# Optimization experiments

Hardware: AMD Instinct MI355X
Metric: run time of the kernel (lower is better)

## Reference

```python
import jax, jax.numpy as jnp
import numpy as np

DIM = 768
NUM_HEADS = 12
HEAD_DIM = DIM // NUM_HEADS
B, V, L = 1, 8, 512


def _block_mask_bias(V, L, dtype):
    # allowed[v_q, v_k]: views 0,1 attend to views 0,1 (incl. self); views >=2 causal (v_q >= v_k)
    vq = jnp.arange(V)[:, None]
    vk = jnp.arange(V)[None, :]
    allowed = ((vq <= 1) & (vk <= 1)) | (vq >= vk)  # [V, V]
    allowed = jnp.repeat(jnp.repeat(allowed, L, axis=0), L, axis=1)  # [V*L, V*L]
    neg_inf = jnp.asarray(-jnp.inf, dtype)
    return jnp.where(allowed, jnp.asarray(0.0, dtype), neg_inf)


def setup_inputs() -> dict:
    key = jax.random.key(0)
    k0, k1, k2, k3, k4, k5 = jax.random.split(key, 6)
    s = 1.0 / np.sqrt(DIM)
    x = jax.random.normal(k0, (B, V, L, DIM), dtype=jnp.float32)
    Wq = jax.random.normal(k1, (DIM, DIM), dtype=jnp.float32) * s
    Wk = jax.random.normal(k2, (DIM, DIM), dtype=jnp.float32) * s
    Wv = jax.random.normal(k3, (DIM, DIM), dtype=jnp.float32) * s
    Wo = jax.random.normal(k4, (DIM, DIM), dtype=jnp.float32) * s
    bo = jax.random.normal(k5, (DIM,), dtype=jnp.float32) * 0.01
    return {"x": x, "Wq": Wq, "Wk": Wk, "Wv": Wv, "Wo": Wo, "bo": bo}


def reference(x, Wq, Wk, Wv, Wo, bo):
    Bx, Vx, Lx, C = x.shape
    S = Vx * Lx
    H, D = NUM_HEADS, HEAD_DIM
    scale = D ** -0.5

    xf = x.reshape(Bx, S, C)
    # linear projections (no bias, qkv_bias=False), split heads -> [B, H, S, D]
    def split_heads(t):
        return t.reshape(Bx, S, H, D).transpose(0, 2, 1, 3)
    q = split_heads(xf @ Wq.T)
    k = split_heads(xf @ Wk.T)
    v = split_heads(xf @ Wv.T)

    bias = _block_mask_bias(Vx, Lx, q.dtype)  # [S, S], broadcast over B, H
    scores = jnp.einsum("bhqd,bhkd->bhqk", q, k) * scale + bias
    attn = jax.nn.softmax(scores, axis=-1)
    out = jnp.einsum("bhqk,bhkd->bhqd", attn, v)  # [B, H, S, D]
    out = out.transpose(0, 2, 1, 3).reshape(Bx, Vx, Lx, C)
    return out @ Wo.T + bo
```

## Files before the change

### kernel.cpp

```cpp
#include <hip/hip_runtime.h>

#define S_TOT 4096
#define C_DIM 768
#define QKV_LD 2304
#define NH 12
#define QSCALE 0.18033688011112042f

using f32x4  = __attribute__((ext_vector_type(4))) float;
using bf16x8 = __attribute__((ext_vector_type(8))) __bf16;

#if __has_builtin(__builtin_amdgcn_exp2f)
#define EXP2(x) __builtin_amdgcn_exp2f(x)
#else
#define EXP2(x) exp2f(x)
#endif

#define DRAIN_AND_BARRIER()                                     \
  do {                                                          \
    asm volatile("s_waitcnt vmcnt(0) lgkmcnt(0)" ::: "memory"); \
    __builtin_amdgcn_sched_barrier(0);                          \
    __syncthreads();                                            \
  } while (0)

__device__ inline unsigned short f2bf_bits(float f) {
  unsigned int u = __float_as_uint(f);
  u = (u + 0x7FFFu + ((u >> 16) & 1u)) >> 16;
  return (unsigned short)u;
}
__device__ inline __bf16 f2bf(float f) {
  unsigned short s = f2bf_bits(f);
  __bf16 b;
  __builtin_memcpy(&b, &s, 2);
  return b;
}

__device__ __forceinline__ void gl_lds16(const __bf16* g, __bf16* l) {
  __builtin_amdgcn_global_load_lds(
      (__attribute__((address_space(1))) void*)(g),
      (__attribute__((address_space(3))) void*)(l), 16, 0, 0);
}

__global__ void cvt_all(const float* __restrict__ x, const float* __restrict__ Wq,
                        const float* __restrict__ Wk, const float* __restrict__ Wv,
                        const float* __restrict__ Wo, __bf16* __restrict__ dst) {
  const int XN = S_TOT * C_DIM;
  const int WN = C_DIM * C_DIM;
  int i = (blockIdx.x * blockDim.x + threadIdx.x) * 4;
  if (i >= XN + 4 * WN) return;
  const float* src; float scale = 1.f; int off;
  if (i < XN)               { src = x;  off = i; }
  else if (i < XN + WN)     { src = Wq; off = i - XN; scale = QSCALE; }
  else if (i < XN + 2 * WN) { src = Wk; off = i - XN - WN; }
  else if (i < XN + 3 * WN) { src = Wv; off = i - XN - 2 * WN; }
  else                      { src = Wo; off = i - XN - 3 * WN; }
  float4 v = *reinterpret_cast<const float4*>(src + off);
  ushort4 o;
  o.x = f2bf_bits(v.x * scale); o.y = f2bf_bits(v.y * scale);
  o.z = f2bf_bits(v.z * scale); o.w = f2bf_bits(v.w * scale);
  *reinterpret_cast<ushort4*>(reinterpret_cast<unsigned short*>(dst) + i) = o;
}

template<bool OUT_BIAS_F32, bool SPLIT_V>
__global__ __launch_bounds__(256) void gemm128(
    const __bf16* __restrict__ A, const __bf16* __restrict__ B,
    void* __restrict__ Cv, const float* __restrict__ bias,
    __bf16* __restrict__ V2, int K, int ldc) {
  __shared__ __bf16 As[128][64];
  __shared__ __bf16 Bs[128][64];
  const int t = threadIdx.x, lane = t & 63, wv = t >> 6;
  const int wr = wv >> 1, wc = wv & 1;
  const int lhi = lane >> 4, llo = lane & 15;
  const int m0 = blockIdx.y * 128, n0 = blockIdx.x * 128;

  f32x4 acc[4][4];
  #pragma unroll
  for (int a = 0; a < 4; ++a)
    #pragma unroll
    for (int b = 0; b < 4; ++b) acc[a][b] = (f32x4){0.f, 0.f, 0.f, 0.f};

  for (int kt = 0; kt < K; kt += 64) {
    __syncthreads();
    #pragma unroll
    for (int n = 0; n < 4; ++n) {
      const int ci = n * 256 + wv * 64 + lane;
      const int r = ci >> 3;
      const int cc = (ci & 7) ^ (r & 7);
      gl_lds16(A + (size_t)(m0 + r) * K + kt + cc * 8, &As[0][0] + ci * 8);
      gl_lds16(B + (size_t)(n0 + r) * K + kt + cc * 8, &Bs[0][0] + ci * 8);
    }
    DRAIN_AND_BARRIER();
    #pragma unroll
    for (int kk = 0; kk < 2; ++kk) {
      bf16x8 af[4], bfr[4];
      #pragma unroll
      for (int mi = 0; mi < 4; ++mi) {
        const int row = wr * 64 + mi * 16 + llo;
        af[mi] = *reinterpret_cast<const bf16x8*>(
            &As[0][0] + row * 64 + (((kk << 2) | lhi) ^ (llo & 7)) * 8);
      }
      #pragma unroll
      for (int ni = 0; ni < 4; ++ni) {
        const int row = wc * 64 + ni * 16 + llo;
        bfr[ni] = *reinterpret_cast<const bf16x8*>(
            &Bs[0][0] + row * 64 + (((kk << 2) | lhi) ^ (llo & 7)) * 8);
      }
      #pragma unroll
      for (int mi = 0; mi < 4; ++mi)
        #pragma unroll
        for (int ni = 0; ni < 4; ++ni)
          acc[mi][ni] = __builtin_amdgcn_mfma_f32_16x16x32_bf16(af[mi], bfr[ni], acc[mi][ni], 0, 0, 0);
    }
  }

  if (SPLIT_V && n0 >= 1536) {
    const int head = (n0 - 1536 + wc * 64) >> 6;
    const int T = (m0 >> 6) + wr;
    #pragma unroll
    for (int mi = 0; mi < 4; ++mi) {
      const int c = (mi >> 1) * 4 + lhi;
      #pragma unroll
      for (int ni = 0; ni < 4; ++ni) {
        const int d = ni * 16 + llo;
        ushort4 o;
        o.x = f2bf_bits(acc[mi][ni][0]); o.y = f2bf_bits(acc[mi][ni][1]);
        o.z = f2bf_bits(acc[mi][ni][2]); o.w = f2bf_bits(acc[mi][ni][3]);
        uint2 u; __builtin_memcpy(&u, &o, 8);
        *reinterpret_cast<uint2*>(
            V2 + ((((size_t)head * 64 + T) * 8 + c) * 64 + d) * 8 + (mi & 1) * 4) = u;
      }
    }
    return;
  }

  #pragma unroll
  for (int mi = 0; mi < 4; ++mi)
    #pragma unroll
    for (int ni = 0; ni < 4; ++ni)
      #pragma unroll
      for (int i = 0; i < 4; ++i) {
        const int row = m0 + wr * 64 + mi * 16 + lhi * 4 + i;
        const int col = n0 + wc * 64 + ni * 16 + llo;
        if constexpr (OUT_BIAS_F32) {
          reinterpret_cast<float*>(Cv)[(size_t)row * ldc + col] = acc[mi][ni][i] + bias[col];
        } else {
          reinterpret_cast<__bf16*>(Cv)[(size_t)row * ldc + col] = f2bf(acc[mi][ni][i]);
        }
      }
}

__device__ __forceinline__ void decode10(int j, int& qb64, int& h, int& nt,
                                         int& kstart, int& slot) {
  if (j < 384) {
    const int c = j & 3, q = (j >> 2) & 7; h = j >> 5;
    qb64 = 56 + q; nt = 16; kstart = c * 1024;
    slot = ((q * 12) + h) * 4 + c;
  } else if (j < 672) {
    const int k = j - 384, c = k % 3, k3 = k / 3, q = k3 & 7; h = k3 >> 3;
    qb64 = 40 + q; nt = 16; kstart = c * 1024;
    slot = 768 + ((q * 12) + h) * 3 + c;
  } else if (j < 864) {
    const int k = j - 672, c = k & 1, q = (k >> 1) & 7; h = k >> 4;
    qb64 = 24 + q; nt = 16; kstart = c * 1024;
    slot = 1344 + ((q * 12) + h) * 2 + c;
  } else if (j < 1056) {
    const int k = j - 864;
    qb64 = k & 15; h = k >> 4; nt = 16; kstart = 0; slot = -1;
  } else if (j < 1440) {
    const int k = j - 1056, c = k & 3, q = (k >> 2) & 7; h = k >> 5;
    qb64 = 48 + q; nt = 14; kstart = c * 896;
    slot = 384 + ((q * 12) + h) * 4 + c;
  } else if (j < 1728) {
    const int k = j - 1440, c = k % 3, k3 = k / 3, q = k3 & 7; h = k3 >> 3;
    qb64 = 32 + q; nt = (c == 0) ? 14 : 13;
    kstart = (c == 0) ? 0 : (896 + (c - 1) * 832);
    slot = 1056 + ((q * 12) + h) * 3 + c;
  } else {
    const int k = j - 1728, c = k & 1, q = (k >> 1) & 7; h = k >> 4;
    qb64 = 16 + q; nt = 12; kstart = c * 768;
    slot = 1536 + ((q * 12) + h) * 2 + c;
  }
}

__global__ __launch_bounds__(256) void attn_fused10(
    const __bf16* __restrict__ QKV, const __bf16* __restrict__ V2,
    __bf16* __restrict__ att, float* __restrict__ Opart,
    float* __restrict__ lpart) {
  __shared__ __bf16 Ks[3][64][64];
  const int t = threadIdx.x, lane = t & 63, wv = t >> 6;
  const int llo = lane & 15, hi = lane >> 4;
  const int sw = llo & 7;
  int qb64, h, n_tiles, kstart, slot;
  decode10((int)blockIdx.x, qb64, h, n_tiles, kstart, slot);
  const int q0 = qb64 * 64;
  const int myq = q0 + wv * 16 + llo;

  bf16x8 qf[2];
  {
    const __bf16* qrow = QKV + (size_t)myq * QKV_LD + h * 64;
    qf[0] = *reinterpret_cast<const bf16x8*>(qrow + hi * 8);
    qf[1] = *reinterpret_cast<const bf16x8*>(qrow + 32 + hi * 8);
  }
  asm volatile("s_waitcnt vmcnt(0)" ::: "memory");

  f32x4 Oa[4];
  #pragma unroll
  for (int dt = 0; dt < 4; ++dt) Oa[dt] = (f32x4){0.f, 0.f, 0.f, 0.f};
  float l = 0.f;

  const int ci0 = (wv * 2 + 0) * 64 + lane, r0 = ci0 >> 3, c0 = (ci0 & 7) ^ (r0 & 7);
  const int ci1 = (wv * 2 + 1) * 64 + lane, r1 = ci1 >> 3, c1 = (ci1 & 7) ^ (r1 & 7);
  const __bf16* kp0 = QKV + (size_t)(kstart + r0) * QKV_LD + C_DIM + h * 64 + c0 * 8;
  const __bf16* kp1 = QKV + (size_t)(kstart + r1) * QKV_LD + C_DIM + h * 64 + c1 * 8;
  __bf16* const kd0 = &Ks[0][0][0] + (wv * 2 + 0) * 512;
  __bf16* const kd1 = &Ks[0][0][0] + (wv * 2 + 1) * 512;

  auto stage = [&](int buf) {
    const size_t bo = (size_t)buf * 4096;
    gl_lds16(kp0, kd0 + bo);
    gl_lds16(kp1, kd1 + bo);
    kp0 += (size_t)64 * QKV_LD; kp1 += (size_t)64 * QKV_LD;
  };

  const __bf16* vg = V2 + ((size_t)(h * 64 + (kstart >> 6))) * 4096 + hi * 512 + llo * 8;

  stage(0);
  stage(1);
  int cur = 0;
  for (int tt = 0; tt < n_tiles; ++tt) {
    if (tt + 1 < n_tiles) {
      asm volatile("s_waitcnt vmcnt(2)" ::: "memory");
    } else {
      asm volatile("s_waitcnt vmcnt(0)" ::: "memory");
    }
    __builtin_amdgcn_sched_barrier(0);
    __builtin_amdgcn_s_barrier();
    __builtin_amdgcn_sched_barrier(0);

    bf16x8 va[4][2];
    #pragma unroll
    for (int dt = 0; dt < 4; ++dt)
      #pragma unroll
      for (int mm = 0; mm < 2; ++mm)
        va[dt][mm] = *reinterpret_cast<const bf16x8*>(vg + mm * 2048 + dt * 128);
    __builtin_amdgcn_sched_barrier(0);

    if (tt + 2 < n_tiles) {
      const int nxt = (cur + 2 >= 3) ? cur - 1 : cur + 2;
      stage(nxt);
    }
    const __bf16* Kb = &Ks[cur][0][0];

    f32x4 sc[4];
    #pragma unroll
    for (int nt = 0; nt < 4; ++nt) sc[nt] = (f32x4){0.f, 0.f, 0.f, 0.f};
    #pragma unroll
    for (int nt = 0; nt < 4; ++nt) {
      const __bf16* kr = Kb + (nt * 16 + llo) * 64;
      bf16x8 kf0 = *reinterpret_cast<const bf16x8*>(kr + ((hi ^ sw) * 8));
      bf16x8 kf1 = *reinterpret_cast<const bf16x8*>(kr + (((4 + hi) ^ sw) * 8));
      sc[nt] = __builtin_amdgcn_mfma_f32_16x16x32_bf16(kf0, qf[0], sc[nt], 0, 0, 0);
      sc[nt] = __builtin_amdgcn_mfma_f32_16x16x32_bf16(kf1, qf[1], sc[nt], 0, 0, 0);
    }

    float pp[4][4];
    #pragma unroll
    for (int nt = 0; nt < 4; ++nt)
      #pragma unroll
      for (int i = 0; i < 4; ++i) pp[nt][i] = EXP2(sc[nt][i]);
    float t0 = (pp[0][0] + pp[0][1]) + (pp[0][2] + pp[0][3]);
    float t1 = (pp[1][0] + pp[1][1]) + (pp[1][2] + pp[1][3]);
    float t2 = (pp[2][0] + pp[2][1]) + (pp[2][2] + pp[2][3]);
    float t3 = (pp[3][0] + pp[3][1]) + (pp[3][2] + pp[3][3]);
    l += (t0 + t1) + (t2 + t3);

    bf16x8 pf[2];
    #pragma unroll
    for (int mm = 0; mm < 2; ++mm)
      #pragma unroll
      for (int jj = 0; jj < 8; ++jj)
        pf[mm][jj] = (__bf16)pp[2 * mm + (jj >> 2)][jj & 3];

    #pragma unroll
    for (int dt = 0; dt < 4; ++dt)
      #pragma unroll
      for (int mm = 0; mm < 2; ++mm)
        Oa[dt] = __builtin_amdgcn_mfma_f32_16x16x32_bf16(va[dt][mm], pf[mm], Oa[dt], 0, 0, 0);

    vg += 4096;
    cur = (cur + 1 == 3) ? 0 : cur + 1;
  }

  l += __shfl_xor(l, 16);
  l += __shfl_xor(l, 32);
  if (slot < 0) {
    const float inv = 1.f / l;
    #pragma unroll
    for (int dt = 0; dt < 4; ++dt) {
      ushort4 o;
      o.x = f2bf_bits(Oa[dt][0] * inv);
      o.y = f2bf_bits(Oa[dt][1] * inv);
      o.z = f2bf_bits(Oa[dt][2] * inv);
      o.w = f2bf_bits(Oa[dt][3] * inv);
      *reinterpret_cast<ushort4*>(att + (size_t)myq * C_DIM + h * 64 + dt * 16 + hi * 4) = o;
    }
  } else {
    float* Ob = Opart + (((size_t)slot * 64) + wv * 16 + llo) * 64;
    #pragma unroll
    for (int dt = 0; dt < 4; ++dt)
      *reinterpret_cast<f32x4*>(Ob + dt * 16 + hi * 4) = Oa[dt];
    if (hi == 0) lpart[slot * 64 + wv * 16 + llo] = l;
  }
}

__global__ __launch_bounds__(256) void merge10(
    const float* __restrict__ Opart, const float* __restrict__ lpart,
    __bf16* __restrict__ att) {
  const int b = blockIdx.x;
  const int qi = b / 12, h = b - qi * 12;
  const int qb64 = 16 + qi;
  int base, n;
  if      (qb64 >= 56) { n = 4; base = ((qb64 - 56) * 12 + h) * 4; }
  else if (qb64 >= 48) { n = 4; base = 384 + ((qb64 - 48) * 12 + h) * 4; }
  else if (qb64 >= 40) { n = 3; base = 768 + ((qb64 - 40) * 12 + h) * 3; }
  else if (qb64 >= 32) { n = 3; base = 1056 + ((qb64 - 32) * 12 + h) * 3; }
  else if (qb64 >= 24) { n = 2; base = 1344 + ((qb64 - 24) * 12 + h) * 2; }
  else                 { n = 2; base = 1536 + ((qb64 - 16) * 12 + h) * 2; }
  const int t = threadIdx.x;
  const int r = t >> 2, d0 = (t & 3) * 16;
  f32x4 s[4] = {{0.f,0.f,0.f,0.f},{0.f,0.f,0.f,0.f},{0.f,0.f,0.f,0.f},{0.f,0.f,0.f,0.f}};
  float L = 0.f;
  for (int k = 0; k < n; ++k) {
    const float* O = Opart + ((size_t)(base + k) * 64 + r) * 64 + d0;
    #pragma unroll
    for (int i = 0; i < 4; ++i) {
      f32x4 v = *reinterpret_cast<const f32x4*>(O + i * 4);
      s[i][0] += v[0]; s[i][1] += v[1]; s[i][2] += v[2]; s[i][3] += v[3];
    }
    L += lpart[(base + k) * 64 + r];
  }
  const float linv = 1.f / L;
  __bf16* dst = att + ((size_t)qb64 * 64 + r) * C_DIM + h * 64 + d0;
  #pragma unroll
  for (int i = 0; i < 4; ++i) {
    ushort4 o;
    o.x = f2bf_bits(s[i][0] * linv);
    o.y = f2bf_bits(s[i][1] * linv);
    o.z = f2bf_bits(s[i][2] * linv);
    o.w = f2bf_bits(s[i][3] * linv);
    *reinterpret_cast<ushort4*>(dst + i * 4) = o;
  }
}

extern "C" void kernel_launch(void* const* d_in, const int* in_sizes, int n_in,
                              void* d_out, int out_size, void* d_ws, size_t ws_size,
                              hipStream_t stream) {
  const float* x  = (const float*)d_in[0];
  const float* Wq = (const float*)d_in[1];
  const float* Wk = (const float*)d_in[2];
  const float* Wv = (const float*)d_in[3];
  const float* Wo = (const float*)d_in[4];
  const float* bo = (const float*)d_in[5];

  __bf16* xb   = (__bf16*)d_ws;
  __bf16* Wqkv = xb + (size_t)S_TOT * C_DIM;
  __bf16* Wob  = Wqkv + (size_t)3 * C_DIM * C_DIM;
  __bf16* QKV  = Wob + (size_t)C_DIM * C_DIM;
  __bf16* V2   = QKV + (size_t)S_TOT * QKV_LD;
  __bf16* att  = V2 + (size_t)NH * 64 * S_TOT;
  float*  Opart = (float*)(att + (size_t)S_TOT * C_DIM);
  float*  lpart = Opart + (size_t)1728 * 64 * 64;

  {
    const int tot = S_TOT * C_DIM + 4 * C_DIM * C_DIM;
    cvt_all<<<dim3((tot / 4 + 255) / 256), dim3(256), 0, stream>>>(
        x, Wq, Wk, Wv, Wo, xb);
  }

  gemm128<false, true><<<dim3(QKV_LD / 128, S_TOT / 128), dim3(256), 0, stream>>>(
      xb, Wqkv, (void*)QKV, nullptr, V2, C_DIM, QKV_LD);

  attn_fused10<<<dim3(1920), dim3(256), 0, stream>>>(QKV, V2, att, Opart, lpart);

  merge10<<<dim3(576), dim3(256), 0, stream>>>(Opart, lpart, att);

  gemm128<true, false><<<dim3(C_DIM / 128, S_TOT / 128), dim3(256), 0, stream>>>(
      att, Wob, d_out, bo, nullptr, C_DIM, C_DIM);
}
```

Measured before the change: 104.5 us.

## Process attention K tiles in pairs with a 4-deep LDS ring

The attention kernel now handles two 64-key tiles per loop iteration, so it needs one workgroup barrier for every two tiles instead of one per tile. The K shared-memory ring grows from 3 to 4 buffers, and the next two tiles are staged together between the two computes. The aim is to cut barrier and wait overhead per tile. In exchange, each iteration waits on all outstanding loads (vmcnt(0)) where it previously waited on vmcnt(2), which shortens the effective prefetch lead. The LDS footprint per block also grows, which may lower occupancy.

```diff
diff --git a/kernel.cpp b/kernel.cpp
--- a/kernel.cpp
+++ b/kernel.cpp
@@ -181,11 +181,11 @@
   }
 }
 
-__global__ __launch_bounds__(256) void attn_fused10(
+__global__ __launch_bounds__(256) void attn_fused11(
     const __bf16* __restrict__ QKV, const __bf16* __restrict__ V2,
     __bf16* __restrict__ att, float* __restrict__ Opart,
     float* __restrict__ lpart) {
-  __shared__ __bf16 Ks[3][64][64];
+  __shared__ __bf16 Ks[4][64][64];
   const int t = threadIdx.x, lane = t & 63, wv = t >> 6;
   const int llo = lane & 15, hi = lane >> 4;
   const int sw = llo & 7;
@@ -223,33 +223,7 @@
 
   const __bf16* vg = V2 + ((size_t)(h * 64 + (kstart >> 6))) * 4096 + hi * 512 + llo * 8;
 
-  stage(0);
-  stage(1);
-  int cur = 0;
-  for (int tt = 0; tt < n_tiles; ++tt) {
-    if (tt + 1 < n_tiles) {
-      asm volatile("s_waitcnt vmcnt(2)" ::: "memory");
-    } else {
-      asm volatile("s_waitcnt vmcnt(0)" ::: "memory");
-    }
-    __builtin_amdgcn_sched_barrier(0);
-    __builtin_amdgcn_s_barrier();
-    __builtin_amdgcn_sched_barrier(0);
-
-    bf16x8 va[4][2];
-    #pragma unroll
-    for (int dt = 0; dt < 4; ++dt)
-      #pragma unroll
-      for (int mm = 0; mm < 2; ++mm)
-        va[dt][mm] = *reinterpret_cast<const bf16x8*>(vg + mm * 2048 + dt * 128);
-    __builtin_amdgcn_sched_barrier(0);
-
-    if (tt + 2 < n_tiles) {
-      const int nxt = (cur + 2 >= 3) ? cur - 1 : cur + 2;
-      stage(nxt);
-    }
-    const __bf16* Kb = &Ks[cur][0][0];
-
+  auto compute = [&](const __bf16* Kb, bf16x8 (&va)[4][2]) {
     f32x4 sc[4];
     #pragma unroll
     for (int nt = 0; nt < 4; ++nt) sc[nt] = (f32x4){0.f, 0.f, 0.f, 0.f};
@@ -261,7 +235,6 @@
       sc[nt] = __builtin_amdgcn_mfma_f32_16x16x32_bf16(kf0, qf[0], sc[nt], 0, 0, 0);
       sc[nt] = __builtin_amdgcn_mfma_f32_16x16x32_bf16(kf1, qf[1], sc[nt], 0, 0, 0);
     }
-
     float pp[4][4];
     #pragma unroll
     for (int nt = 0; nt < 4; ++nt)
@@ -272,22 +245,57 @@
     float t2 = (pp[2][0] + pp[2][1]) + (pp[2][2] + pp[2][3]);
     float t3 = (pp[3][0] + pp[3][1]) + (pp[3][2] + pp[3][3]);
     l += (t0 + t1) + (t2 + t3);
-
     bf16x8 pf[2];
     #pragma unroll
     for (int mm = 0; mm < 2; ++mm)
       #pragma unroll
       for (int jj = 0; jj < 8; ++jj)
         pf[mm][jj] = (__bf16)pp[2 * mm + (jj >> 2)][jj & 3];
-
     #pragma unroll
     for (int dt = 0; dt < 4; ++dt)
       #pragma unroll
       for (int mm = 0; mm < 2; ++mm)
         Oa[dt] = __builtin_amdgcn_mfma_f32_16x16x32_bf16(va[dt][mm], pf[mm], Oa[dt], 0, 0, 0);
-
-    vg += 4096;
-    cur = (cur + 1 == 3) ? 0 : cur + 1;
+  };
+
+  stage(0);
+  stage(1);
+  int cur = 0;
+  int tt = 0;
+  while (tt < n_tiles) {
+    const bool pair = (tt + 1 < n_tiles);
+    asm volatile("s_waitcnt vmcnt(0)" ::: "memory");
+    __builtin_amdgcn_sched_barrier(0);
+    __builtin_amdgcn_s_barrier();
+    __builtin_amdgcn_sched_barrier(0);
+
+    bf16x8 va0[4][2];
+    #pragma unroll
+    for (int dt = 0; dt < 4; ++dt)
+      #pragma unroll
+      for (int mm = 0; mm < 2; ++mm)
+        va0[dt][mm] = *reinterpret_cast<const bf16x8*>(vg + mm * 2048 + dt * 128);
+    __builtin_amdgcn_sched_barrier(0);
+
+    compute(&Ks[cur][0][0], va0);
+
+    if (pair) {
+      bf16x8 va1[4][2];
+      #pragma unroll
+      for (int dt = 0; dt < 4; ++dt)
+        #pragma unroll
+        for (int mm = 0; mm < 2; ++mm)
+          va1[dt][mm] = *reinterpret_cast<const bf16x8*>(vg + 4096 + mm * 2048 + dt * 128);
+      __builtin_amdgcn_sched_barrier(0);
+      if (tt + 2 < n_tiles) stage((cur + 2) & 3);
+      if (tt + 3 < n_tiles) stage((cur + 3) & 3);
+      __builtin_amdgcn_sched_barrier(0);
+
+      compute(&Ks[(cur + 1) & 3][0][0], va1);
+      vg += 8192; tt += 2; cur = (cur + 2) & 3;
+    } else {
+      vg += 4096; tt += 1; cur = (cur + 1) & 3;
+    }
   }
 
   l += __shfl_xor(l, 16);
@@ -379,7 +387,7 @@
   gemm128<false, true><<<dim3(QKV_LD / 128, S_TOT / 128), dim3(256), 0, stream>>>(
       xb, Wqkv, (void*)QKV, nullptr, V2, C_DIM, QKV_LD);
 
-  attn_fused10<<<dim3(1920), dim3(256), 0, stream>>>(QKV, V2, att, Opart, lpart);
+  attn_fused11<<<dim3(1920), dim3(256), 0, stream>>>(QKV, V2, att, Opart, lpart);
 
   merge10<<<dim3(576), dim3(256), 0, stream>>>(Opart, lpart, att);
 
```

Result: no change. 103.6 us (-0.8%).

## Double attention query tile to 128 rows with 8-wave blocks and new split schedule

Applied to the files above, without the earlier changes.

The attention kernel moves from 64-query, 4-wave blocks to 128-query, 8-wave blocks, so each staged K tile in shared memory is reused by twice as many query rows. Each thread now issues one K load per stage instead of two, and the wait count is simplified accordingly. The work decomposition and split-K slot table are redone for 1056 blocks, and the merge kernel is updated to match. The aim is less K traffic and staging overhead per query, at the cost of coarser load balancing, fewer blocks and higher register/LDS pressure per block.

```diff
diff --git a/kernel.cpp b/kernel.cpp
--- a/kernel.cpp
+++ b/kernel.cpp
@@ -148,40 +148,40 @@
       }
 }
 
-__device__ __forceinline__ void decode10(int j, int& qb64, int& h, int& nt,
+__device__ __forceinline__ void decode13(int j, int& qb, int& h, int& nt,
                                          int& kstart, int& slot) {
-  if (j < 384) {
-    const int c = j & 3, q = (j >> 2) & 7; h = j >> 5;
-    qb64 = 56 + q; nt = 16; kstart = c * 1024;
-    slot = ((q * 12) + h) * 4 + c;
-  } else if (j < 672) {
-    const int k = j - 384, c = k % 3, k3 = k / 3, q = k3 & 7; h = k3 >> 3;
-    qb64 = 40 + q; nt = 16; kstart = c * 1024;
-    slot = 768 + ((q * 12) + h) * 3 + c;
-  } else if (j < 864) {
-    const int k = j - 672, c = k & 1, q = (k >> 1) & 7; h = k >> 4;
-    qb64 = 24 + q; nt = 16; kstart = c * 1024;
-    slot = 1344 + ((q * 12) + h) * 2 + c;
-  } else if (j < 1056) {
-    const int k = j - 864;
-    qb64 = k & 15; h = k >> 4; nt = 16; kstart = 0; slot = -1;
-  } else if (j < 1440) {
-    const int k = j - 1056, c = k & 3, q = (k >> 2) & 7; h = k >> 5;
-    qb64 = 48 + q; nt = 14; kstart = c * 896;
-    slot = 384 + ((q * 12) + h) * 4 + c;
-  } else if (j < 1728) {
-    const int k = j - 1440, c = k % 3, k3 = k / 3, q = k3 & 7; h = k3 >> 3;
-    qb64 = 32 + q; nt = (c == 0) ? 14 : 13;
+  if (j < 96) {
+    const int c = j & 1, u = j >> 1;
+    qb = 12 + (u & 3); h = u >> 2; nt = 16; kstart = c * 1024;
+    slot = ((u & 3) * 12 + h) * 2 + c;
+  } else if (j < 192) {
+    const int k = j - 96;
+    qb = k & 7; h = k >> 3; nt = 16; kstart = 0; slot = -1;
+  } else if (j < 384) {
+    const int k = j - 192, c = k & 3, u = k >> 2;
+    qb = 24 + (u & 3); h = u >> 2; nt = 14; kstart = c * 896;
+    slot = 96 + ((u & 3) * 12 + h) * 4 + c;
+  } else if (j < 624) {
+    const int k = j - 384, c = k % 5, u = k / 5;
+    qb = 28 + (u & 3); h = u >> 2; nt = (c < 4) ? 13 : 12; kstart = c * 832;
+    slot = 288 + ((u & 3) * 12 + h) * 5 + c;
+  } else if (j < 768) {
+    const int k = j - 624, c = k % 3, u = k / 3;
+    qb = 16 + (u & 3); h = u >> 2; nt = (c == 0) ? 14 : 13;
     kstart = (c == 0) ? 0 : (896 + (c - 1) * 832);
-    slot = 1056 + ((q * 12) + h) * 3 + c;
+    slot = 528 + ((u & 3) * 12 + h) * 3 + c;
+  } else if (j < 960) {
+    const int k = j - 768, c = k & 3, u = k >> 2;
+    qb = 20 + (u & 3); h = u >> 2; nt = 12; kstart = c * 768;
+    slot = 672 + ((u & 3) * 12 + h) * 4 + c;
   } else {
-    const int k = j - 1728, c = k & 1, q = (k >> 1) & 7; h = k >> 4;
-    qb64 = 16 + q; nt = 12; kstart = c * 768;
-    slot = 1536 + ((q * 12) + h) * 2 + c;
-  }
-}
-
-__global__ __launch_bounds__(256) void attn_fused10(
+    const int k = j - 960, c = k & 1, u = k >> 1;
+    qb = 8 + (u & 3); h = u >> 2; nt = 12; kstart = c * 768;
+    slot = 864 + ((u & 3) * 12 + h) * 2 + c;
+  }
+}
+
+__global__ __launch_bounds__(512) void attn_fused13(
     const __bf16* __restrict__ QKV, const __bf16* __restrict__ V2,
     __bf16* __restrict__ att, float* __restrict__ Opart,
     float* __restrict__ lpart) {
@@ -189,10 +189,9 @@
   const int t = threadIdx.x, lane = t & 63, wv = t >> 6;
   const int llo = lane & 15, hi = lane >> 4;
   const int sw = llo & 7;
-  int qb64, h, n_tiles, kstart, slot;
-  decode10((int)blockIdx.x, qb64, h, n_tiles, kstart, slot);
-  const int q0 = qb64 * 64;
-  const int myq = q0 + wv * 16 + llo;
+  int qb, h, n_tiles, kstart, slot;
+  decode13((int)blockIdx.x, qb, h, n_tiles, kstart, slot);
+  const int myq = qb * 128 + wv * 16 + llo;
 
   bf16x8 qf[2];
   {
@@ -207,18 +206,14 @@
   for (int dt = 0; dt < 4; ++dt) Oa[dt] = (f32x4){0.f, 0.f, 0.f, 0.f};
   float l = 0.f;
 
-  const int ci0 = (wv * 2 + 0) * 64 + lane, r0 = ci0 >> 3, c0 = (ci0 & 7) ^ (r0 & 7);
-  const int ci1 = (wv * 2 + 1) * 64 + lane, r1 = ci1 >> 3, c1 = (ci1 & 7) ^ (r1 & 7);
-  const __bf16* kp0 = QKV + (size_t)(kstart + r0) * QKV_LD + C_DIM + h * 64 + c0 * 8;
-  const __bf16* kp1 = QKV + (size_t)(kstart + r1) * QKV_LD + C_DIM + h * 64 + c1 * 8;
-  __bf16* const kd0 = &Ks[0][0][0] + (wv * 2 + 0) * 512;
-  __bf16* const kd1 = &Ks[0][0][0] + (wv * 2 + 1) * 512;
+  const int r = t >> 3;
+  const int cc = (t & 7) ^ (r & 7);
+  const __bf16* kp = QKV + (size_t)(kstart + r) * QKV_LD + C_DIM + h * 64 + cc * 8;
+  __bf16* const kd = &Ks[0][0][0] + (size_t)wv * 512;
 
   auto stage = [&](int buf) {
-    const size_t bo = (size_t)buf * 4096;
-    gl_lds16(kp0, kd0 + bo);
-    gl_lds16(kp1, kd1 + bo);
-    kp0 += (size_t)64 * QKV_LD; kp1 += (size_t)64 * QKV_LD;
+    gl_lds16(kp, kd + (size_t)buf * 4096);
+    kp += (size_t)64 * QKV_LD;
   };
 
   const __bf16* vg = V2 + ((size_t)(h * 64 + (kstart >> 6))) * 4096 + hi * 512 + llo * 8;
@@ -227,11 +222,7 @@
   stage(1);
   int cur = 0;
   for (int tt = 0; tt < n_tiles; ++tt) {
-    if (tt + 1 < n_tiles) {
-      asm volatile("s_waitcnt vmcnt(2)" ::: "memory");
-    } else {
-      asm volatile("s_waitcnt vmcnt(0)" ::: "memory");
-    }
+    asm volatile("s_waitcnt vmcnt(1)" ::: "memory");
     __builtin_amdgcn_sched_barrier(0);
     __builtin_amdgcn_s_barrier();
     __builtin_amdgcn_sched_barrier(0);
@@ -304,42 +295,43 @@
       *reinterpret_cast<ushort4*>(att + (size_t)myq * C_DIM + h * 64 + dt * 16 + hi * 4) = o;
     }
   } else {
-    float* Ob = Opart + (((size_t)slot * 64) + wv * 16 + llo) * 64;
+    const int rloc = wv * 16 + llo;
+    float* Ob = Opart + ((size_t)slot * 128 + rloc) * 64;
     #pragma unroll
     for (int dt = 0; dt < 4; ++dt)
       *reinterpret_cast<f32x4*>(Ob + dt * 16 + hi * 4) = Oa[dt];
-    if (hi == 0) lpart[slot * 64 + wv * 16 + llo] = l;
-  }
-}
-
-__global__ __launch_bounds__(256) void merge10(
+    if (hi == 0) lpart[slot * 128 + rloc] = l;
+  }
+}
+
+__global__ __launch_bounds__(512) void merge13(
     const float* __restrict__ Opart, const float* __restrict__ lpart,
     __bf16* __restrict__ att) {
   const int b = blockIdx.x;
   const int qi = b / 12, h = b - qi * 12;
-  const int qb64 = 16 + qi;
+  const int qb = 8 + qi;
   int base, n;
-  if      (qb64 >= 56) { n = 4; base = ((qb64 - 56) * 12 + h) * 4; }
-  else if (qb64 >= 48) { n = 4; base = 384 + ((qb64 - 48) * 12 + h) * 4; }
-  else if (qb64 >= 40) { n = 3; base = 768 + ((qb64 - 40) * 12 + h) * 3; }
-  else if (qb64 >= 32) { n = 3; base = 1056 + ((qb64 - 32) * 12 + h) * 3; }
-  else if (qb64 >= 24) { n = 2; base = 1344 + ((qb64 - 24) * 12 + h) * 2; }
-  else                 { n = 2; base = 1536 + ((qb64 - 16) * 12 + h) * 2; }
+  if      (qb >= 28) { n = 5; base = 288 + ((qb - 28) * 12 + h) * 5; }
+  else if (qb >= 24) { n = 4; base = 96 + ((qb - 24) * 12 + h) * 4; }
+  else if (qb >= 20) { n = 4; base = 672 + ((qb - 20) * 12 + h) * 4; }
+  else if (qb >= 16) { n = 3; base = 528 + ((qb - 16) * 12 + h) * 3; }
+  else if (qb >= 12) { n = 2; base = 0 + ((qb - 12) * 12 + h) * 2; }
+  else               { n = 2; base = 864 + ((qb - 8) * 12 + h) * 2; }
   const int t = threadIdx.x;
   const int r = t >> 2, d0 = (t & 3) * 16;
   f32x4 s[4] = {{0.f,0.f,0.f,0.f},{0.f,0.f,0.f,0.f},{0.f,0.f,0.f,0.f},{0.f,0.f,0.f,0.f}};
   float L = 0.f;
   for (int k = 0; k < n; ++k) {
-    const float* O = Opart + ((size_t)(base + k) * 64 + r) * 64 + d0;
+    const float* O = Opart + ((size_t)(base + k) * 128 + r) * 64 + d0;
     #pragma unroll
     for (int i = 0; i < 4; ++i) {
       f32x4 v = *reinterpret_cast<const f32x4*>(O + i * 4);
       s[i][0] += v[0]; s[i][1] += v[1]; s[i][2] += v[2]; s[i][3] += v[3];
     }
-    L += lpart[(base + k) * 64 + r];
+    L += lpart[(base + k) * 128 + r];
   }
   const float linv = 1.f / L;
-  __bf16* dst = att + ((size_t)qb64 * 64 + r) * C_DIM + h * 64 + d0;
+  __bf16* dst = att + ((size_t)qb * 128 + r) * C_DIM + h * 64 + d0;
   #pragma unroll
   for (int i = 0; i < 4; ++i) {
     ushort4 o;
@@ -368,7 +360,7 @@
   __bf16* V2   = QKV + (size_t)S_TOT * QKV_LD;
   __bf16* att  = V2 + (size_t)NH * 64 * S_TOT;
   float*  Opart = (float*)(att + (size_t)S_TOT * C_DIM);
-  float*  lpart = Opart + (size_t)1728 * 64 * 64;
+  float*  lpart = Opart + (size_t)960 * 128 * 64;
 
   {
     const int tot = S_TOT * C_DIM + 4 * C_DIM * C_DIM;
@@ -379,9 +371,9 @@
   gemm128<false, true><<<dim3(QKV_LD / 128, S_TOT / 128), dim3(256), 0, stream>>>(
       xb, Wqkv, (void*)QKV, nullptr, V2, C_DIM, QKV_LD);
 
-  attn_fused10<<<dim3(1920), dim3(256), 0, stream>>>(QKV, V2, att, Opart, lpart);
-
-  merge10<<<dim3(576), dim3(256), 0, stream>>>(Opart, lpart, att);
+  attn_fused13<<<dim3(1056), dim3(512), 0, stream>>>(QKV, V2, att, Opart, lpart);
+
+  merge13<<<dim3(288), dim3(512), 0, stream>>>(Opart, lpart, att);
 
   gemm128<true, false><<<dim3(C_DIM / 128, S_TOT / 128), dim3(256), 0, stream>>>(
       att, Wob, d_out, bo, nullptr, C_DIM, C_DIM);
```

Result: slower. 110.8 us (+6.1%).
